# Kernel optimization log

Hardware: AMD Instinct MI355X
Metric: run time of the kernel (lower is better)

Reference implementation:

```python
import jax, jax.numpy as jnp
import numpy as np

B, S, D = 32, 2048, 1024

def setup_inputs() -> dict:
    key = jax.random.key(0)
    k1, k2, k3, k4, k5 = jax.random.split(key, 5)
    st = jax.random.normal(k1, (B, D), dtype=jnp.float32)
    hx = jax.random.normal(k2, (B, S, D), dtype=jnp.float32)
    hx_mask = (jax.random.uniform(k3, (B, S)) < 0.9).astype(jnp.float32)
    # kaiming_normal_(a=1, fan_in) -> std = sqrt(2/(1+a^2)/fan_in) = 1/sqrt(D)
    W = jax.random.normal(k4, (D, D), dtype=jnp.float32) / jnp.sqrt(jnp.float32(D))
    b = jax.random.normal(k5, (D,), dtype=jnp.float32)
    return {"st": st, "hx": hx, "hx_mask": hx_mask, "W": W, "b": b}

def reference(st, hx, hx_mask, W, b):
    # attn_type == 'general', prior_att is None
    # multiplicative mask with 1e-18 epsilon (faithful to original)
    hx_mask1 = hx_mask + (1.0 - hx_mask) * 1e-18            # [B,S]
    hx_t = jnp.einsum('bsd,ed->bse', hx, W) + b             # linear on hx, [B,S,D]
    score = jnp.einsum('bsd,bd->bs', hx_t, st)              # bmm(hx_t, st)
    score = score * hx_mask1
    attn = jax.nn.softmax(score, axis=-1)                   # [B,S]
    ct = jnp.einsum('bs,bsd->bd', attn, hx_t)               # weighted sum over src_len
    return ct
```

## Files before the change

kernel.cpp:

```cpp
#include <hip/hip_runtime.h>
#include <math.h>

#define BB 32
#define SS 2048
#define DD 1024
#define CHUNKS 32
#define ROWS_PER_CHUNK (SS / CHUNKS)
#define NWAVES 4
#define ROWS_PER_WAVE (ROWS_PER_CHUNK / NWAVES)
#define PSTRIDE (DD + 4)

#define ESPL 8
#define EPB (DD / ESPL)
#define VBG 8
#define VBPG (BB / VBG)

typedef float f32x4 __attribute__((ext_vector_type(4)));

__device__ __forceinline__ f32x4 ldnt4(const float* p) {
    return __builtin_nontemporal_load(reinterpret_cast<const f32x4*>(p));
}
__device__ __forceinline__ f32x4 ld4(const float* p) {
    return *reinterpret_cast<const f32x4*>(p);
}

__global__ __launch_bounds__(256) void k_v(const float* __restrict__ st,
                                           const float* __restrict__ W,
                                           float* __restrict__ part_v) {
    const int dchunk = blockIdx.x;
    const int es = blockIdx.y;
    const int bg = blockIdx.z;
    const int tid = threadIdx.x;
    const int d = dchunk * 256 + tid;
    const int e0 = es * EPB;
    const int b0 = bg * VBPG;

    __shared__ float st_s[VBPG][EPB];
    for (int i = tid; i < VBPG * EPB; i += 256)
        st_s[i >> 7][i & 127] = st[(b0 + (i >> 7)) * DD + e0 + (i & 127)];
    __syncthreads();

    float acc[VBPG];
#pragma unroll
    for (int j = 0; j < VBPG; ++j) acc[j] = 0.f;

    for (int e = 0; e < EPB; ++e) {
        const float w = W[(size_t)(e0 + e) * DD + d];
#pragma unroll
        for (int j = 0; j < VBPG; ++j) acc[j] += st_s[j][e] * w;
    }
#pragma unroll
    for (int j = 0; j < VBPG; ++j)
        part_v[((size_t)es * BB + b0 + j) * DD + d] = acc[j];
}

__global__ __launch_bounds__(256, 4) void k_main(const float* __restrict__ hx,
                                                 const float* __restrict__ mask,
                                                 const float* __restrict__ part_v,
                                                 const float* __restrict__ st,
                                                 const float* __restrict__ bias,
                                                 float* __restrict__ part) {
    const int chunk = blockIdx.x;
    const int b = blockIdx.y;
    const int tid = threadIdx.x;
    const int wave = tid >> 6;
    const int lane = tid & 63;

    f32x4 vr[4];
#pragma unroll
    for (int k = 0; k < 4; ++k) vr[k] = (f32x4)(0.f);
#pragma unroll
    for (int es = 0; es < ESPL; ++es) {
        const float* pv = part_v + ((size_t)es * BB + b) * DD + 4 * lane;
#pragma unroll
        for (int k = 0; k < 4; ++k) vr[k] += ld4(pv + k * 256);
    }

    float cb = 0.f;
    {
        const float* stb = st + b * DD + 4 * lane;
        const float* bb = bias + 4 * lane;
#pragma unroll
        for (int k = 0; k < 4; ++k) {
            f32x4 bv = ld4(bb + k * 256);
            f32x4 sv = ld4(stb + k * 256);
            cb += bv.x * sv.x + bv.y * sv.y + bv.z * sv.z + bv.w * sv.w;
        }
#pragma unroll
        for (int o = 32; o; o >>= 1) cb += __shfl_xor(cb, o, 64);
    }

    const int s0 = chunk * ROWS_PER_CHUNK + wave * ROWS_PER_WAVE;
    const float* hxb = hx + (size_t)b * SS * DD + 4 * lane;
    const float* mb = mask + (size_t)b * SS;

    float m = -INFINITY, l = 0.f;
    f32x4 u[4];
#pragma unroll
    for (int k = 0; k < 4; ++k) u[k] = (f32x4)(0.f);

    f32x4 hA[2][4], hB[2][4];

    auto loadrows = [&](f32x4 (&h)[2][4], int s) {
        const float* r0 = hxb + (size_t)s * DD;
#pragma unroll
        for (int k = 0; k < 4; ++k) {
            h[0][k] = ldnt4(r0 + k * 256);
            h[1][k] = ldnt4(r0 + DD + k * 256);
        }
    };

    auto compute = [&](const f32x4 (&h)[2][4], int s) {
        float d0 = 0.f, d1 = 0.f;
#pragma unroll
        for (int k = 0; k < 4; ++k) {
            d0 += h[0][k].x * vr[k].x + h[0][k].y * vr[k].y + h[0][k].z * vr[k].z + h[0][k].w * vr[k].w;
            d1 += h[1][k].x * vr[k].x + h[1][k].y * vr[k].y + h[1][k].z * vr[k].z + h[1][k].w * vr[k].w;
        }
        const bool odd = (lane & 1);
        float a = odd ? d1 : d0;
        float t = odd ? d0 : d1;
        a += __shfl_xor(t, 1, 64);
        a += __shfl_xor(a, 2, 64);
        a += __shfl_xor(a, 4, 64);
        a += __shfl_xor(a, 8, 64);
        a += __shfl_xor(a, 16, 64);
        a += __shfl_xor(a, 32, 64);
        const float o = __shfl_xor(a, 1, 64);
        const float dd0 = odd ? o : a;
        const float dd1 = odd ? a : o;

        const float2 mk = *reinterpret_cast<const float2*>(mb + s);
        const float sc0 = (dd0 + cb) * (mk.x + (1.0f - mk.x) * 1e-18f);
        const float sc1 = (dd1 + cb) * (mk.y + (1.0f - mk.y) * 1e-18f);

        const float gm = fmaxf(sc0, sc1);
        if (gm > m) {
            const float f = __expf(m - gm);
            l *= f;
#pragma unroll
            for (int k = 0; k < 4; ++k) u[k] *= f;
            m = gm;
        }
        const float p0 = __expf(sc0 - m);
        const float p1 = __expf(sc1 - m);
        l += p0 + p1;
#pragma unroll
        for (int k = 0; k < 4; ++k) u[k] += p0 * h[0][k] + p1 * h[1][k];
    };

    loadrows(hA, s0);
#pragma unroll
    for (int g = 0; g < ROWS_PER_WAVE / 2 - 1; ++g) {
        if (g & 1) { loadrows(hA, s0 + 2 * (g + 1)); compute(hB, s0 + 2 * g); }
        else       { loadrows(hB, s0 + 2 * (g + 1)); compute(hA, s0 + 2 * g); }
    }
    compute(hB, s0 + ROWS_PER_WAVE - 2);

    __shared__ float s_m[NWAVES], s_l[NWAVES];
    __shared__ float s_u[NWAVES][DD];
    if (lane == 0) { s_m[wave] = m; s_l[wave] = l; }
#pragma unroll
    for (int k = 0; k < 4; ++k)
        *reinterpret_cast<f32x4*>(&s_u[wave][k * 256 + 4 * lane]) = u[k];
    __syncthreads();

    const float M = fmaxf(fmaxf(s_m[0], s_m[1]), fmaxf(s_m[2], s_m[3]));
    const float f0 = __expf(s_m[0] - M), f1 = __expf(s_m[1] - M);
    const float f2 = __expf(s_m[2] - M), f3 = __expf(s_m[3] - M);
    const float L = s_l[0] * f0 + s_l[1] * f1 + s_l[2] * f2 + s_l[3] * f3;

    float* pb = part + (size_t)(b * CHUNKS + chunk) * PSTRIDE;
    f32x4 a0 = ld4(&s_u[0][4 * tid]);
    f32x4 a1 = ld4(&s_u[1][4 * tid]);
    f32x4 a2 = ld4(&s_u[2][4 * tid]);
    f32x4 a3 = ld4(&s_u[3][4 * tid]);
    f32x4 acc = a0 * f0 + a1 * f1 + a2 * f2 + a3 * f3;
    *reinterpret_cast<f32x4*>(pb + 4 * tid) = acc;
    if (tid == 0) { pb[DD] = M; pb[DD + 1] = L; }
}

__global__ __launch_bounds__(256) void k_reduce(const float* __restrict__ part,
                                                float* __restrict__ ubar) {
    const int b = blockIdx.x;
    const int tid = threadIdx.x;
    __shared__ float s_f[CHUNKS];
    __shared__ float s_red[2];
    const float* pb = part + (size_t)b * CHUNKS * PSTRIDE;

    float mi = (tid < CHUNKS) ? pb[tid * PSTRIDE + DD] : -INFINITY;
    float M = mi;
#pragma unroll
    for (int o = 32; o; o >>= 1) M = fmaxf(M, __shfl_xor(M, o, 64));
    if (tid == 0) s_red[0] = M;
    __syncthreads();
    M = s_red[0];

    const float li = (tid < CHUNKS) ? pb[tid * PSTRIDE + DD + 1] : 0.f;
    const float fi = (tid < CHUNKS) ? __expf(mi - M) : 0.f;
    if (tid < CHUNKS) s_f[tid] = fi;
    float Lp = li * fi;
#pragma unroll
    for (int o = 32; o; o >>= 1) Lp += __shfl_xor(Lp, o, 64);
    if (tid == 0) s_red[1] = Lp;
    __syncthreads();
    const float invL = 1.f / s_red[1];

    f32x4 acc = (f32x4)(0.f);
    for (int i = 0; i < CHUNKS; ++i) {
        const float f = s_f[i];
        f32x4 ui = ld4(pb + (size_t)i * PSTRIDE + 4 * tid);
        acc += f * ui;
    }
    acc *= invL;
    *reinterpret_cast<f32x4*>(ubar + (size_t)b * DD + 4 * tid) = acc;
}

__global__ __launch_bounds__(256) void k_out(const float* __restrict__ ubar,
                                             const float* __restrict__ W,
                                             const float* __restrict__ bias,
                                             float* __restrict__ out) {
    const int echunk = blockIdx.x;
    const int bg = blockIdx.y;
    const int tid = threadIdx.x;
    const int wave = tid >> 6;
    const int lane = tid & 63;
    const int b0 = bg * 4;

    f32x4 ur[4][4];
#pragma unroll
    for (int j = 0; j < 4; ++j) {
        const float* ub = ubar + (size_t)(b0 + j) * DD + 4 * lane;
#pragma unroll
        for (int k = 0; k < 4; ++k) ur[j][k] = ld4(ub + k * 256);
    }

    for (int i = 0; i < 4; ++i) {
        const int e = echunk * 16 + wave * 4 + i;
        const float* wr = W + (size_t)e * DD + 4 * lane;
        f32x4 w4[4];
#pragma unroll
        for (int k = 0; k < 4; ++k) w4[k] = ld4(wr + k * 256);

        float d0 = 0.f, d1 = 0.f, d2 = 0.f, d3 = 0.f;
#pragma unroll
        for (int k = 0; k < 4; ++k) {
            d0 += w4[k].x * ur[0][k].x + w4[k].y * ur[0][k].y + w4[k].z * ur[0][k].z + w4[k].w * ur[0][k].w;
            d1 += w4[k].x * ur[1][k].x + w4[k].y * ur[1][k].y + w4[k].z * ur[1][k].z + w4[k].w * ur[1][k].w;
            d2 += w4[k].x * ur[2][k].x + w4[k].y * ur[2][k].y + w4[k].z * ur[2][k].z + w4[k].w * ur[2][k].w;
            d3 += w4[k].x * ur[3][k].x + w4[k].y * ur[3][k].y + w4[k].z * ur[3][k].z + w4[k].w * ur[3][k].w;
        }
#pragma unroll
        for (int o = 32; o; o >>= 1) {
            d0 += __shfl_xor(d0, o, 64);
            d1 += __shfl_xor(d1, o, 64);
            d2 += __shfl_xor(d2, o, 64);
            d3 += __shfl_xor(d3, o, 64);
        }
        if (lane == 0) {
            const float be = bias[e];
            out[(size_t)(b0 + 0) * DD + e] = d0 + be;
            out[(size_t)(b0 + 1) * DD + e] = d1 + be;
            out[(size_t)(b0 + 2) * DD + e] = d2 + be;
            out[(size_t)(b0 + 3) * DD + e] = d3 + be;
        }
    }
}

extern "C" void kernel_launch(void* const* d_in, const int* in_sizes, int n_in,
                              void* d_out, int out_size, void* d_ws, size_t ws_size,
                              hipStream_t stream) {
    const float* st   = (const float*)d_in[0];
    const float* hx   = (const float*)d_in[1];
    const float* msk  = (const float*)d_in[2];
    const float* W    = (const float*)d_in[3];
    const float* bias = (const float*)d_in[4];
    float* out = (float*)d_out;

    float* ws = (float*)d_ws;
    float* part_v = ws;
    float* part   = part_v + (size_t)ESPL * BB * DD;
    float* ubar   = part + (size_t)BB * CHUNKS * PSTRIDE;

    k_v<<<dim3(4, ESPL, VBG), 256, 0, stream>>>(st, W, part_v);
    k_main<<<dim3(CHUNKS, BB), 256, 0, stream>>>(hx, msk, part_v, st, bias, part);
    k_reduce<<<BB, 256, 0, stream>>>(part, ubar);
    k_out<<<dim3(64, 8), 256, 0, stream>>>(ubar, W, bias, out);
}
```

Measured before the change: 69.99 us.

## Fuse chunk reduction into output GEMV kernel and batch W loads in k_v

Merges the k_reduce and k_out kernels into one k_tail kernel. Each block recomputes the per-batch softmax merge across chunks into shared memory, then multiplies by a slice of W with four rows per iteration. This removes one kernel launch and the ubar round trip through global memory. The cost is that the chunk reduction is repeated ECH=8 times per batch and W is re-read per batch instead of shared across four batches. k_v also loads eight W values before the FMA loop to raise memory-level parallelism.

Result: slower. 78.32 us (+11.9%).

```diff
diff --git a/kernel.cpp b/kernel.cpp
--- a/kernel.cpp
+++ b/kernel.cpp
@@ -14,6 +14,9 @@
 #define EPB (DD / ESPL)
 #define VBG 8
 #define VBPG (BB / VBG)
+
+#define ECH 8
+#define EPB_OUT (DD / ECH)
 
 typedef float f32x4 __attribute__((ext_vector_type(4)));
 
@@ -44,10 +47,16 @@
 #pragma unroll
     for (int j = 0; j < VBPG; ++j) acc[j] = 0.f;
 
-    for (int e = 0; e < EPB; ++e) {
-        const float w = W[(size_t)(e0 + e) * DD + d];
-#pragma unroll
-        for (int j = 0; j < VBPG; ++j) acc[j] += st_s[j][e] * w;
+    const float* Wd = W + d;
+    for (int e = 0; e < EPB; e += 8) {
+        float w[8];
+#pragma unroll
+        for (int q = 0; q < 8; ++q)
+            w[q] = Wd[(size_t)(e0 + e + q) * DD];
+#pragma unroll
+        for (int q = 0; q < 8; ++q)
+#pragma unroll
+            for (int j = 0; j < VBPG; ++j) acc[j] += st_s[j][e + q] * w[q];
     }
 #pragma unroll
     for (int j = 0; j < VBPG; ++j)
@@ -180,75 +189,64 @@
     if (tid == 0) { pb[DD] = M; pb[DD + 1] = L; }
 }
 
-__global__ __launch_bounds__(256) void k_reduce(const float* __restrict__ part,
-                                                float* __restrict__ ubar) {
-    const int b = blockIdx.x;
-    const int tid = threadIdx.x;
-    __shared__ float s_f[CHUNKS];
-    __shared__ float s_red[2];
-    const float* pb = part + (size_t)b * CHUNKS * PSTRIDE;
-
-    float mi = (tid < CHUNKS) ? pb[tid * PSTRIDE + DD] : -INFINITY;
-    float M = mi;
-#pragma unroll
-    for (int o = 32; o; o >>= 1) M = fmaxf(M, __shfl_xor(M, o, 64));
-    if (tid == 0) s_red[0] = M;
-    __syncthreads();
-    M = s_red[0];
-
-    const float li = (tid < CHUNKS) ? pb[tid * PSTRIDE + DD + 1] : 0.f;
-    const float fi = (tid < CHUNKS) ? __expf(mi - M) : 0.f;
-    if (tid < CHUNKS) s_f[tid] = fi;
-    float Lp = li * fi;
-#pragma unroll
-    for (int o = 32; o; o >>= 1) Lp += __shfl_xor(Lp, o, 64);
-    if (tid == 0) s_red[1] = Lp;
-    __syncthreads();
-    const float invL = 1.f / s_red[1];
-
-    f32x4 acc = (f32x4)(0.f);
-    for (int i = 0; i < CHUNKS; ++i) {
-        const float f = s_f[i];
-        f32x4 ui = ld4(pb + (size_t)i * PSTRIDE + 4 * tid);
-        acc += f * ui;
-    }
-    acc *= invL;
-    *reinterpret_cast<f32x4*>(ubar + (size_t)b * DD + 4 * tid) = acc;
-}
-
-__global__ __launch_bounds__(256) void k_out(const float* __restrict__ ubar,
-                                             const float* __restrict__ W,
-                                             const float* __restrict__ bias,
-                                             float* __restrict__ out) {
-    const int echunk = blockIdx.x;
-    const int bg = blockIdx.y;
+__global__ __launch_bounds__(256) void k_tail(const float* __restrict__ part,
+                                              const float* __restrict__ W,
+                                              const float* __restrict__ bias,
+                                              float* __restrict__ out) {
+    const int ec = blockIdx.x;
+    const int b = blockIdx.y;
     const int tid = threadIdx.x;
     const int wave = tid >> 6;
     const int lane = tid & 63;
-    const int b0 = bg * 4;
-
-    f32x4 ur[4][4];
-#pragma unroll
-    for (int j = 0; j < 4; ++j) {
-        const float* ub = ubar + (size_t)(b0 + j) * DD + 4 * lane;
-#pragma unroll
-        for (int k = 0; k < 4; ++k) ur[j][k] = ld4(ub + k * 256);
-    }
-
-    for (int i = 0; i < 4; ++i) {
-        const int e = echunk * 16 + wave * 4 + i;
+    const float* pb = part + (size_t)b * CHUNKS * PSTRIDE;
+
+    __shared__ float s_f[CHUNKS];
+    __shared__ float ubar_s[DD];
+
+    const float mi = (lane < CHUNKS) ? pb[lane * PSTRIDE + DD] : -INFINITY;
+    float M = mi;
+#pragma unroll
+    for (int o = 32; o; o >>= 1) M = fmaxf(M, __shfl_xor(M, o, 64));
+    const float li = (lane < CHUNKS) ? pb[lane * PSTRIDE + DD + 1] : 0.f;
+    const float fi = (lane < CHUNKS) ? __expf(mi - M) : 0.f;
+    float L = li * fi;
+#pragma unroll
+    for (int o = 32; o; o >>= 1) L += __shfl_xor(L, o, 64);
+    if (wave == 0 && lane < CHUNKS) s_f[lane] = fi;
+    __syncthreads();
+    const float invL = 1.f / L;
+
+    f32x4 acc = (f32x4)(0.f);
+#pragma unroll
+    for (int i = 0; i < CHUNKS; ++i)
+        acc += s_f[i] * ld4(pb + (size_t)i * PSTRIDE + 4 * tid);
+    acc *= invL;
+    *reinterpret_cast<f32x4*>(&ubar_s[4 * tid]) = acc;
+    __syncthreads();
+
+    f32x4 ur[4];
+#pragma unroll
+    for (int k = 0; k < 4; ++k) ur[k] = ld4(&ubar_s[k * 256 + 4 * lane]);
+
+    const int ebase = ec * EPB_OUT + wave * (EPB_OUT / NWAVES);
+    for (int i = 0; i < 8; ++i) {
+        const int e = ebase + 4 * i;
+        f32x4 w0[4], w1[4], w2[4], w3[4];
         const float* wr = W + (size_t)e * DD + 4 * lane;
-        f32x4 w4[4];
-#pragma unroll
-        for (int k = 0; k < 4; ++k) w4[k] = ld4(wr + k * 256);
-
+#pragma unroll
+        for (int k = 0; k < 4; ++k) {
+            w0[k] = ld4(wr + k * 256);
+            w1[k] = ld4(wr + DD + k * 256);
+            w2[k] = ld4(wr + 2 * DD + k * 256);
+            w3[k] = ld4(wr + 3 * DD + k * 256);
+        }
         float d0 = 0.f, d1 = 0.f, d2 = 0.f, d3 = 0.f;
 #pragma unroll
         for (int k = 0; k < 4; ++k) {
-            d0 += w4[k].x * ur[0][k].x + w4[k].y * ur[0][k].y + w4[k].z * ur[0][k].z + w4[k].w * ur[0][k].w;
-            d1 += w4[k].x * ur[1][k].x + w4[k].y * ur[1][k].y + w4[k].z * ur[1][k].z + w4[k].w * ur[1][k].w;
-            d2 += w4[k].x * ur[2][k].x + w4[k].y * ur[2][k].y + w4[k].z * ur[2][k].z + w4[k].w * ur[2][k].w;
-            d3 += w4[k].x * ur[3][k].x + w4[k].y * ur[3][k].y + w4[k].z * ur[3][k].z + w4[k].w * ur[3][k].w;
+            d0 += w0[k].x * ur[k].x + w0[k].y * ur[k].y + w0[k].z * ur[k].z + w0[k].w * ur[k].w;
+            d1 += w1[k].x * ur[k].x + w1[k].y * ur[k].y + w1[k].z * ur[k].z + w1[k].w * ur[k].w;
+            d2 += w2[k].x * ur[k].x + w2[k].y * ur[k].y + w2[k].z * ur[k].z + w2[k].w * ur[k].w;
+            d3 += w3[k].x * ur[k].x + w3[k].y * ur[k].y + w3[k].z * ur[k].z + w3[k].w * ur[k].w;
         }
 #pragma unroll
         for (int o = 32; o; o >>= 1) {
@@ -258,11 +256,10 @@
             d3 += __shfl_xor(d3, o, 64);
         }
         if (lane == 0) {
-            const float be = bias[e];
-            out[(size_t)(b0 + 0) * DD + e] = d0 + be;
-            out[(size_t)(b0 + 1) * DD + e] = d1 + be;
-            out[(size_t)(b0 + 2) * DD + e] = d2 + be;
-            out[(size_t)(b0 + 3) * DD + e] = d3 + be;
+            out[(size_t)b * DD + e + 0] = d0 + bias[e + 0];
+            out[(size_t)b * DD + e + 1] = d1 + bias[e + 1];
+            out[(size_t)b * DD + e + 2] = d2 + bias[e + 2];
+            out[(size_t)b * DD + e + 3] = d3 + bias[e + 3];
         }
     }
 }
@@ -280,10 +277,8 @@
     float* ws = (float*)d_ws;
     float* part_v = ws;
     float* part   = part_v + (size_t)ESPL * BB * DD;
-    float* ubar   = part + (size_t)BB * CHUNKS * PSTRIDE;
 
     k_v<<<dim3(4, ESPL, VBG), 256, 0, stream>>>(st, W, part_v);
     k_main<<<dim3(CHUNKS, BB), 256, 0, stream>>>(hx, msk, part_v, st, bias, part);
-    k_reduce<<<BB, 256, 0, stream>>>(part, ubar);
-    k_out<<<dim3(64, 8), 256, 0, stream>>>(ubar, W, bias, out);
-}
+    k_tail<<<dim3(ECH, BB), 256, 0, stream>>>(part, W, bias, out);
+}
```
